# Kernel tuning notes

Measured on AMD Instinct MI355X. Metric: run time of the kernel, lower is better.

## Reference

```python
import jax, jax.numpy as jnp
import numpy as np

B, T, D_MODEL = 2, 2048, 1024
N_HEAD, D_HEAD = 16, 64
EPS = 1e-5


def setup_inputs() -> dict:
    key = jax.random.key(0)
    ks = jax.random.split(key, 6)
    s = 0.02  # init scale
    x = jax.random.normal(ks[0], (B, T, D_MODEL), jnp.float32)
    Wq = jax.random.normal(ks[1], (D_MODEL, N_HEAD * D_HEAD), jnp.float32) * s
    Wk = jax.random.normal(ks[2], (D_MODEL, N_HEAD * D_HEAD), jnp.float32) * s
    Wv = jax.random.normal(ks[3], (D_MODEL, N_HEAD * D_HEAD), jnp.float32) * s
    Wo = jax.random.normal(ks[4], (N_HEAD * D_HEAD, D_MODEL), jnp.float32) * s
    bo = jnp.zeros((D_MODEL,), jnp.float32)
    gamma = jnp.ones((D_MODEL,), jnp.float32)
    beta = jnp.zeros((D_MODEL,), jnp.float32)
    # causal mask: True = masked out (matches masked_fill semantics)
    mask = jnp.triu(jnp.ones((T, T), dtype=bool), k=1)[None, None]  # [1,1,T,T]
    return {"x": x, "Wq": Wq, "Wk": Wk, "Wv": Wv, "Wo": Wo, "bo": bo,
            "gamma": gamma, "beta": beta, "mask": mask}


def reference(x, Wq, Wk, Wv, Wo, bo, gamma, beta, mask):
    B_, T_, D = x.shape
    # pre-LayerNorm (biased variance, eps=1e-5, matching torch)
    mu = jnp.mean(x, axis=-1, keepdims=True)
    var = jnp.mean(jnp.square(x - mu), axis=-1, keepdims=True)
    xn = (x - mu) / jnp.sqrt(var + EPS) * gamma + beta
    # QKV projections (no bias)
    q = (xn @ Wq).reshape(B_, T_, N_HEAD, D_HEAD)
    k = (xn @ Wk).reshape(B_, T_, N_HEAD, D_HEAD)
    v = (xn @ Wv).reshape(B_, T_, N_HEAD, D_HEAD)
    scale = 1.0 / (D_HEAD ** 0.5)
    scores = jnp.einsum('bthd,bshd->bhts', q, k) * scale  # [B,H,T,T]
    scores = jnp.where(mask, -jnp.finfo(scores.dtype).max, scores)
    attn = jax.nn.softmax(scores, axis=-1)
    o = jnp.einsum('bhts,bshd->bthd', attn, v).reshape(B_, T_, N_HEAD * D_HEAD)
    out = o @ Wo + bo  # dropout is identity (eval / p=0)
    # pre_layernorm=True: residual uses the NORMALIZED x (faithful to source)
    return xn + out
```

## Files before the change

kernel.cpp:

```cpp
#include <hip/hip_runtime.h>
#include <hip/hip_bf16.h>

typedef unsigned short u16;
typedef __attribute__((ext_vector_type(8))) short bf16x8;
typedef __attribute__((ext_vector_type(4))) float f32x4;

#define T_SEQ 2048
#define DM 1024
#define NH 16
#define DH 64

__device__ __forceinline__ float bf2f(u16 u) {
  return __uint_as_float(((unsigned int)u) << 16);
}
__device__ __forceinline__ u16 f2bf(float f) {
  unsigned int u = __float_as_uint(f);
  u += 0x7fff + ((u >> 16) & 1);
  return (u16)(u >> 16);
}
__device__ __forceinline__ bool in_is_f32(const void* gamma) {
  return ((const u16*)gamma)[0] != 0x3F80;
}

__global__ __launch_bounds__(256) void ln_k(const void* __restrict__ x,
                                            const void* __restrict__ gamma,
                                            const void* __restrict__ beta,
                                            u16* __restrict__ xn,
                                            float2* __restrict__ stats) {
  bool f32 = in_is_f32(gamma);
  int row = blockIdx.x;
  int t = threadIdx.x;
  float v[4];
  if (f32) {
    float4 u = ((const float4*)((const float*)x + (size_t)row * DM))[t];
    v[0] = u.x; v[1] = u.y; v[2] = u.z; v[3] = u.w;
  } else {
    uint2 u = ((const uint2*)((const u16*)x + (size_t)row * DM))[t];
    v[0] = bf2f((u16)(u.x & 0xffff)); v[1] = bf2f((u16)(u.x >> 16));
    v[2] = bf2f((u16)(u.y & 0xffff)); v[3] = bf2f((u16)(u.y >> 16));
  }
  float s = v[0] + v[1] + v[2] + v[3];
  float ss = v[0]*v[0] + v[1]*v[1] + v[2]*v[2] + v[3]*v[3];
  #pragma unroll
  for (int m = 1; m < 64; m <<= 1) {
    s += __shfl_xor(s, m);
    ss += __shfl_xor(ss, m);
  }
  __shared__ float red[8];
  int wid = t >> 6;
  if ((t & 63) == 0) { red[wid] = s; red[4 + wid] = ss; }
  __syncthreads();
  float S = red[0] + red[1] + red[2] + red[3];
  float SS = red[4] + red[5] + red[6] + red[7];
  float mu = S * (1.0f / DM);
  float var = SS * (1.0f / DM) - mu * mu;
  float rstd = rsqrtf(var + 1e-5f);
  if (t == 0) stats[row] = make_float2(mu, rstd);
  float gv[4], bv[4];
  if (f32) {
    float4 ug = ((const float4*)gamma)[t];
    float4 ub = ((const float4*)beta)[t];
    gv[0] = ug.x; gv[1] = ug.y; gv[2] = ug.z; gv[3] = ug.w;
    bv[0] = ub.x; bv[1] = ub.y; bv[2] = ub.z; bv[3] = ub.w;
  } else {
    uint2 ug = ((const uint2*)gamma)[t];
    uint2 ub = ((const uint2*)beta)[t];
    gv[0] = bf2f((u16)(ug.x & 0xffff)); gv[1] = bf2f((u16)(ug.x >> 16));
    gv[2] = bf2f((u16)(ug.y & 0xffff)); gv[3] = bf2f((u16)(ug.y >> 16));
    bv[0] = bf2f((u16)(ub.x & 0xffff)); bv[1] = bf2f((u16)(ub.x >> 16));
    bv[2] = bf2f((u16)(ub.y & 0xffff)); bv[3] = bf2f((u16)(ub.y >> 16));
  }
  u16 o[4];
  #pragma unroll
  for (int i = 0; i < 4; i++) o[i] = f2bf((v[i] - mu) * rstd * gv[i] + bv[i]);
  uint2 w;
  w.x = (unsigned)o[0] | ((unsigned)o[1] << 16);
  w.y = (unsigned)o[2] | ((unsigned)o[3] << 16);
  *(uint2*)&xn[(size_t)row * DM + t * 4] = w;
}

__global__ __launch_bounds__(256) void transp_cvt(const void* __restrict__ W0,
                                                  const void* __restrict__ W1,
                                                  const void* __restrict__ W2,
                                                  const void* __restrict__ W3,
                                                  u16* __restrict__ out,
                                                  const void* __restrict__ gamma) {
  bool f32 = in_is_f32(gamma);
  int z = blockIdx.z;
  const void* in = (z == 0) ? W0 : (z == 1) ? W1 : (z == 2) ? W2 : W3;
  u16* dst0 = out + (size_t)z * 1024 * 1024;
  __shared__ __align__(16) u16 tile[64][72];
  int c0 = blockIdx.x * 64, r0 = blockIdx.y * 64;
  int t = threadIdx.x;
  int rr = t >> 2, seg = t & 3;
  u16 w[16];
  if (f32) {
    const float4* p = (const float4*)((const float*)in + (size_t)(r0 + rr) * 1024 + c0 + seg * 16);
    float4 q0 = p[0], q1 = p[1], q2 = p[2], q3 = p[3];
    w[0] = f2bf(q0.x);  w[1] = f2bf(q0.y);  w[2] = f2bf(q0.z);  w[3] = f2bf(q0.w);
    w[4] = f2bf(q1.x);  w[5] = f2bf(q1.y);  w[6] = f2bf(q1.z);  w[7] = f2bf(q1.w);
    w[8] = f2bf(q2.x);  w[9] = f2bf(q2.y);  w[10] = f2bf(q2.z); w[11] = f2bf(q2.w);
    w[12] = f2bf(q3.x); w[13] = f2bf(q3.y); w[14] = f2bf(q3.z); w[15] = f2bf(q3.w);
  } else {
    const u16* p = (const u16*)in + (size_t)(r0 + rr) * 1024 + c0 + seg * 16;
    bf16x8 a0 = *(const bf16x8*)p;
    bf16x8 a1 = *(const bf16x8*)(p + 8);
    #pragma unroll
    for (int i = 0; i < 8; i++) { w[i] = (u16)a0[i]; w[8 + i] = (u16)a1[i]; }
  }
  #pragma unroll
  for (int i = 0; i < 16; i++) tile[rr][seg * 16 + i] = w[i];
  __syncthreads();
  u16 vals[16];
  #pragma unroll
  for (int i = 0; i < 16; i++) vals[i] = tile[seg * 16 + i][rr];
  u16* dst = &dst0[(size_t)(c0 + rr) * 1024 + r0 + seg * 16];
  #pragma unroll
  for (int q = 0; q < 4; q++) {
    ushort4 p4;
    p4.x = vals[4 * q]; p4.y = vals[4 * q + 1]; p4.z = vals[4 * q + 2]; p4.w = vals[4 * q + 3];
    *(ushort4*)(dst + 4 * q) = p4;
  }
}

template<int TM, int LDA>
__global__ __launch_bounds__(256) void gemm_k(const u16* __restrict__ A,
                                              const u16* __restrict__ BT,
                                              u16* __restrict__ Cq,
                                              u16* __restrict__ vt,
                                              void* __restrict__ Cout,
                                              const void* __restrict__ bo,
                                              const void* __restrict__ x,
                                              const void* __restrict__ gamma,
                                              const void* __restrict__ beta,
                                              const float2* __restrict__ stats,
                                              int mode) {
  constexpr int NI = (TM == 128) ? 4 : 1;
  constexpr int NJ = (TM == 128) ? 4 : 8;
  constexpr int ACH = (TM == 128) ? 2 : 1;
  __shared__ __align__(16) u16 As[TM * 32];
  __shared__ __align__(16) u16 Bs[128 * 32];
  const int K = 1024;
  int tid = threadIdx.x;
  int lane = tid & 63, wid = tid >> 6;
  int wm = (TM == 128) ? (wid >> 1) : wid;
  int wn = (TM == 128) ? (wid & 1) : 0;
  int m0 = blockIdx.x * TM, n0 = blockIdx.y * 128;
  int quad = lane >> 4, lcol = lane & 15;
  bool vmode = (mode == 0) && (n0 >= 2048);

  f32x4 acc[NI][NJ];
  #pragma unroll
  for (int i = 0; i < NI; i++)
    #pragma unroll
    for (int j = 0; j < NJ; j++) acc[i][j] = (f32x4){0.f, 0.f, 0.f, 0.f};

  int srow = tid >> 2, scol = (tid & 3) * 8;
  const u16* Ag0 = A + (size_t)(m0 + srow) * LDA + scol;
  const u16* Ag1 = A + (size_t)(m0 + 64 + srow) * LDA + scol;
  const u16* Bg0 = BT + (size_t)(n0 + srow) * 1024 + scol;
  const u16* Bg1 = BT + (size_t)(n0 + 64 + srow) * 1024 + scol;

  uint4 pa0 = *(const uint4*)Ag0;
  uint4 pa1;
  if (ACH == 2) pa1 = *(const uint4*)Ag1;
  uint4 pb0 = *(const uint4*)Bg0;
  uint4 pb1 = *(const uint4*)Bg1;

  for (int k0 = 0; k0 < K; k0 += 32) {
    if (k0) __syncthreads();
    *(uint4*)(As + tid * 8) = pa0;
    if (ACH == 2) *(uint4*)(As + 2048 + tid * 8) = pa1;
    *(uint4*)(Bs + tid * 8) = pb0;
    *(uint4*)(Bs + 2048 + tid * 8) = pb1;
    __syncthreads();
    if (k0 + 32 < K) {
      pa0 = *(const uint4*)(Ag0 + k0 + 32);
      if (ACH == 2) pa1 = *(const uint4*)(Ag1 + k0 + 32);
      pb0 = *(const uint4*)(Bg0 + k0 + 32);
      pb1 = *(const uint4*)(Bg1 + k0 + 32);
    }
    bf16x8 af[NI], bfr[NJ];
    #pragma unroll
    for (int i = 0; i < NI; i++) {
      int row = (TM == 128) ? (wm * 64 + i * 16 + lcol) : (wm * 16 + lcol);
      af[i] = *(const bf16x8*)&As[row * 32 + quad * 8];
    }
    #pragma unroll
    for (int j = 0; j < NJ; j++) {
      int col = ((TM == 128) ? wn * 64 : 0) + j * 16 + lcol;
      bfr[j] = *(const bf16x8*)&Bs[col * 32 + quad * 8];
    }
    if (vmode) {
      #pragma unroll
      for (int i = 0; i < NI; i++)
        #pragma unroll
        for (int j = 0; j < NJ; j++)
          acc[i][j] = __builtin_amdgcn_mfma_f32_16x16x32_bf16(af[i], bfr[j], acc[i][j], 0, 0, 0);
    } else {
      #pragma unroll
      for (int i = 0; i < NI; i++)
        #pragma unroll
        for (int j = 0; j < NJ; j++)
          acc[i][j] = __builtin_amdgcn_mfma_f32_16x16x32_bf16(bfr[j], af[i], acc[i][j], 0, 0, 0);
    }
  }

  if (mode == 0) {
    if (!vmode) {
      #pragma unroll
      for (int i = 0; i < NI; i++) {
        int m = m0 + ((TM == 128) ? wm * 64 + i * 16 : wm * 16) + lcol;
        #pragma unroll
        for (int j = 0; j < NJ; j++) {
          int nb2 = n0 + ((TM == 128) ? wn * 64 : 0) + j * 16 + quad * 4;
          ushort4 p;
          p.x = f2bf(acc[i][j][0]); p.y = f2bf(acc[i][j][1]);
          p.z = f2bf(acc[i][j][2]); p.w = f2bf(acc[i][j][3]);
          *(ushort4*)&Cq[(size_t)m * 2048 + nb2] = p;
        }
      }
    } else {
      #pragma unroll
      for (int i = 0; i < NI; i++)
        #pragma unroll
        for (int j = 0; j < NJ; j++) {
          int c = n0 - 2048 + ((TM == 128) ? wn * 64 : 0) + j * 16 + lcol;
          int h = c >> 6, d = c & 63;
          int tb = m0 + ((TM == 128) ? wm * 64 + i * 16 : wm * 16) + quad * 4;
          int bb = tb >> 11, tt = tb & 2047;
          ushort4 p;
          p.x = f2bf(acc[i][j][0]); p.y = f2bf(acc[i][j][1]);
          p.z = f2bf(acc[i][j][2]); p.w = f2bf(acc[i][j][3]);
          *(ushort4*)&vt[((size_t)(bb * NH + h) * DH + d) * T_SEQ + tt] = p;
        }
    }
  } else {
    bool f32 = in_is_f32(gamma);
    #pragma unroll
    for (int i = 0; i < NI; i++) {
      int m = m0 + ((TM == 128) ? wm * 64 + i * 16 : wm * 16) + lcol;
      float2 st = stats[m];
      #pragma unroll
      for (int j = 0; j < NJ; j++) {
        int nb2 = n0 + ((TM == 128) ? wn * 64 : 0) + j * 16 + quad * 4;
        size_t idx = (size_t)m * DM + nb2;
        float g4[4], b4[4], bo4[4], x4[4];
        if (f32) {
          float4 g = *(const float4*)((const float*)gamma + nb2);
          float4 be = *(const float4*)((const float*)beta + nb2);
          float4 bb = *(const float4*)((const float*)bo + nb2);
          float4 xv = *(const float4*)((const float*)x + idx);
          g4[0]=g.x; g4[1]=g.y; g4[2]=g.z; g4[3]=g.w;
          b4[0]=be.x; b4[1]=be.y; b4[2]=be.z; b4[3]=be.w;
          bo4[0]=bb.x; bo4[1]=bb.y; bo4[2]=bb.z; bo4[3]=bb.w;
          x4[0]=xv.x; x4[1]=xv.y; x4[2]=xv.z; x4[3]=xv.w;
        } else {
          const u16* gp = (const u16*)gamma + nb2;
          const u16* bp = (const u16*)beta + nb2;
          const u16* op = (const u16*)bo + nb2;
          const u16* xp = (const u16*)x + idx;
          #pragma unroll
          for (int r = 0; r < 4; r++) {
            g4[r] = bf2f(gp[r]); b4[r] = bf2f(bp[r]);
            bo4[r] = bf2f(op[r]); x4[r] = bf2f(xp[r]);
          }
        }
        float o4[4];
        #pragma unroll
        for (int r = 0; r < 4; r++) {
          float xnv = (x4[r] - st.x) * st.y * g4[r] + b4[r];
          o4[r] = acc[i][j][r] + bo4[r] + xnv;
        }
        if (f32) {
          float4 o; o.x = o4[0]; o.y = o4[1]; o.z = o4[2]; o.w = o4[3];
          *(float4*)((float*)Cout + idx) = o;
        } else {
          ushort4 o;
          o.x = f2bf(o4[0]); o.y = f2bf(o4[1]); o.z = f2bf(o4[2]); o.w = f2bf(o4[3]);
          *(ushort4*)((u16*)Cout + idx) = o;
        }
      }
    }
  }
}

__global__ __launch_bounds__(256) void attn(const u16* __restrict__ qk,
                                            const u16* __restrict__ vt,
                                            u16* __restrict__ o) {
  __shared__ __align__(16) u16 Ks[64 * 72];
  __shared__ __align__(16) u16 Vs[64 * 72];
  __shared__ __align__(16) u16 Psm[4][16 * 72];
  int tid = threadIdx.x;
  int lane = tid & 63, wid = tid >> 6;
  int bh = blockIdx.y;
  int b = bh >> 4, h = bh & 15;
  int quad = lane >> 4, lcol = lane & 15;
  int r0 = tid >> 3, seg8 = (tid & 7) * 8;

  const u16* Kbase = qk + (size_t)(b * T_SEQ) * 2048 + 1024 + h * DH;
  const u16* Vbase = vt + (size_t)(b * NH + h) * DH * T_SEQ;

  #pragma unroll
  for (int pi = 0; pi < 2; pi++) {
    int qt = pi ? (int)blockIdx.x : 31 - (int)blockIdx.x;
    int q0 = qt * 64 + wid * 16;
    const u16* qrow = qk + ((size_t)(b * T_SEQ) + q0 + lcol) * 2048 + h * DH + quad * 8;
    bf16x8 qa0 = *(const bf16x8*)(qrow);
    bf16x8 qa1 = *(const bf16x8*)(qrow + 32);

    f32x4 Oacc[4];
    #pragma unroll
    for (int jd = 0; jd < 4; jd++) Oacc[jd] = (f32x4){0.f, 0.f, 0.f, 0.f};
    float lpart[4] = {0.f, 0.f, 0.f, 0.f};
    int ktmax = qt * 64;

    uint4 kp0 = *(const uint4*)(Kbase + (size_t)r0 * 2048 + seg8);
    uint4 kp1 = *(const uint4*)(Kbase + (size_t)(r0 + 32) * 2048 + seg8);
    uint4 vp0 = *(const uint4*)(Vbase + (size_t)r0 * 2048 + seg8);
    uint4 vp1 = *(const uint4*)(Vbase + (size_t)(r0 + 32) * 2048 + seg8);

    for (int kt = 0; kt <= ktmax; kt += 64) {
      __syncthreads();
      *(uint4*)&Ks[r0 * 72 + seg8] = kp0;
      *(uint4*)&Ks[(r0 + 32) * 72 + seg8] = kp1;
      *(uint4*)&Vs[r0 * 72 + seg8] = vp0;
      *(uint4*)&Vs[(r0 + 32) * 72 + seg8] = vp1;
      __syncthreads();
      if (kt < ktmax) {
        int kn = kt + 64;
        kp0 = *(const uint4*)(Kbase + (size_t)(kn + r0) * 2048 + seg8);
        kp1 = *(const uint4*)(Kbase + (size_t)(kn + r0 + 32) * 2048 + seg8);
        vp0 = *(const uint4*)(Vbase + (size_t)r0 * 2048 + kn + seg8);
        vp1 = *(const uint4*)(Vbase + (size_t)(r0 + 32) * 2048 + kn + seg8);
      }
      f32x4 S[4];
      #pragma unroll
      for (int j = 0; j < 4; j++) {
        bf16x8 kb0 = *(const bf16x8*)&Ks[(j * 16 + lcol) * 72 + quad * 8];
        bf16x8 kb1 = *(const bf16x8*)&Ks[(j * 16 + lcol) * 72 + 32 + quad * 8];
        f32x4 s = (f32x4){0.f, 0.f, 0.f, 0.f};
        s = __builtin_amdgcn_mfma_f32_16x16x32_bf16(qa0, kb0, s, 0, 0, 0);
        s = __builtin_amdgcn_mfma_f32_16x16x32_bf16(qa1, kb1, s, 0, 0, 0);
        S[j] = s;
      }
      if (kt < ktmax) {
        #pragma unroll
        for (int r = 0; r < 4; r++) {
          float rs = 0.f;
          #pragma unroll
          for (int j = 0; j < 4; j++) {
            float p = __expf(S[j][r] * 0.125f);
            S[j][r] = p;
            rs += p;
          }
          lpart[r] += rs;
        }
      } else {
        #pragma unroll
        for (int r = 0; r < 4; r++) {
          int qg = q0 + quad * 4 + r;
          float rs = 0.f;
          #pragma unroll
          for (int j = 0; j < 4; j++) {
            int key = kt + j * 16 + lcol;
            float p = (key <= qg) ? __expf(S[j][r] * 0.125f) : 0.f;
            S[j][r] = p;
            rs += p;
          }
          lpart[r] += rs;
        }
      }
      #pragma unroll
      for (int j = 0; j < 4; j++)
        #pragma unroll
        for (int r = 0; r < 4; r++)
          Psm[wid][(quad * 4 + r) * 72 + j * 16 + lcol] = f2bf(S[j][r]);
      #pragma unroll
      for (int s = 0; s < 2; s++) {
        bf16x8 pa = *(const bf16x8*)&Psm[wid][lcol * 72 + s * 32 + quad * 8];
        #pragma unroll
        for (int jd = 0; jd < 4; jd++) {
          bf16x8 vb = *(const bf16x8*)&Vs[(jd * 16 + lcol) * 72 + s * 32 + quad * 8];
          Oacc[jd] = __builtin_amdgcn_mfma_f32_16x16x32_bf16(pa, vb, Oacc[jd], 0, 0, 0);
        }
      }
    }
    #pragma unroll
    for (int r = 0; r < 4; r++) {
      float rs = lpart[r];
      rs += __shfl_xor(rs, 1);
      rs += __shfl_xor(rs, 2);
      rs += __shfl_xor(rs, 4);
      rs += __shfl_xor(rs, 8);
      float inv = 1.0f / rs;
      int qg = q0 + quad * 4 + r;
      size_t rowbase = ((size_t)(b * T_SEQ) + qg) * 2048 + h * DH;
      #pragma unroll
      for (int jd = 0; jd < 4; jd++)
        o[rowbase + jd * 16 + lcol] = f2bf(Oacc[jd][r] * inv);
    }
  }
}

extern "C" void kernel_launch(void* const* d_in, const int* in_sizes, int n_in,
                              void* d_out, int out_size, void* d_ws, size_t ws_size,
                              hipStream_t stream) {
  (void)in_sizes; (void)n_in; (void)out_size; (void)ws_size;
  const void* x     = d_in[0];
  const void* Wq    = d_in[1];
  const void* Wk    = d_in[2];
  const void* Wv    = d_in[3];
  const void* Wo    = d_in[4];
  const void* bo    = d_in[5];
  const void* gamma = d_in[6];
  const void* beta  = d_in[7];

  u16* ws = (u16*)d_ws;
  u16* xn  = ws;
  u16* qkb = xn + (size_t)4096 * 1024;
  u16* vt  = qkb + (size_t)4096 * 2048;
  u16* WT  = vt + (size_t)2 * 16 * 64 * 2048;
  float2* stats = (float2*)(WT + (size_t)4096 * 1024);
  u16* WoT = WT + (size_t)3 * 1024 * 1024;

  ln_k<<<4096, 256, 0, stream>>>(x, gamma, beta, xn, stats);

  transp_cvt<<<dim3(16, 16, 4), 256, 0, stream>>>(Wq, Wk, Wv, Wo, WT, gamma);

  gemm_k<128, 1024><<<dim3(32, 24), 256, 0, stream>>>(xn, WT, qkb, vt, nullptr,
                                                      nullptr, nullptr, gamma,
                                                      nullptr, nullptr, 0);

  attn<<<dim3(16, 32), 256, 0, stream>>>(qkb, vt, qkb);

  gemm_k<64, 2048><<<dim3(64, 8), 256, 0, stream>>>(qkb, WoT, nullptr, nullptr,
                                                    d_out, bo, x, gamma, beta,
                                                    stats, 1);
}
```

Measured before the change: 235.7 us.

## Split attention key tile across waves and keep P in registers via transposed MFMA

The attention block now splits each 64-key tile across its four waves instead of splitting the queries. Each wave computes S transposed (K as the A operand, Q as B) so the exp'd probabilities land directly in the 16x16x16 MFMA operand layout for P·V. This removes the per-wave P round trip through shared memory. The cost is that each wave now holds partial O accumulators for all 64 queries, which means a cross-wave reduction through shared memory, with extra syncs, at the end. Register use roughly quadruples for Oacc, which may reduce occupancy.

```diff
diff --git a/kernel.cpp b/kernel.cpp
--- a/kernel.cpp
+++ b/kernel.cpp
@@ -3,6 +3,7 @@
 
 typedef unsigned short u16;
 typedef __attribute__((ext_vector_type(8))) short bf16x8;
+typedef __attribute__((ext_vector_type(4))) short bf16x4;
 typedef __attribute__((ext_vector_type(4))) float f32x4;
 
 #define T_SEQ 2048
@@ -20,6 +21,16 @@
 }
 __device__ __forceinline__ bool in_is_f32(const void* gamma) {
   return ((const u16*)gamma)[0] != 0x3F80;
+}
+__device__ __forceinline__ f32x4 mfma16(bf16x4 a, bf16x4 b, f32x4 c) {
+#if __has_builtin(__builtin_amdgcn_mfma_f32_16x16x16bf16_1k)
+  return __builtin_amdgcn_mfma_f32_16x16x16bf16_1k(a, b, c, 0, 0, 0);
+#else
+  f32x4 d;
+  asm volatile("v_mfma_f32_16x16x16_bf16 %0, %1, %2, %3\n\ts_nop 7\n\ts_nop 2"
+               : "=v"(d) : "v"(a), "v"(b), "v"(c));
+  return d;
+#endif
 }
 
 __global__ __launch_bounds__(256) void ln_k(const void* __restrict__ x,
@@ -288,9 +299,11 @@
 __global__ __launch_bounds__(256) void attn(const u16* __restrict__ qk,
                                             const u16* __restrict__ vt,
                                             u16* __restrict__ o) {
-  __shared__ __align__(16) u16 Ks[64 * 72];
-  __shared__ __align__(16) u16 Vs[64 * 72];
-  __shared__ __align__(16) u16 Psm[4][16 * 72];
+  __shared__ __align__(16) unsigned char smem[64 * 72 * 2 * 2];
+  __shared__ float Lbuf[4][4][16];
+  u16* Ks = (u16*)smem;
+  u16* Vs = Ks + 64 * 72;
+  float* Ob = (float*)smem;
   int tid = threadIdx.x;
   int lane = tid & 63, wid = tid >> 6;
   int bh = blockIdx.y;
@@ -303,102 +316,102 @@
 
   #pragma unroll
   for (int pi = 0; pi < 2; pi++) {
-    int qt = pi ? (int)blockIdx.x : 31 - (int)blockIdx.x;
-    int q0 = qt * 64 + wid * 16;
-    const u16* qrow = qk + ((size_t)(b * T_SEQ) + q0 + lcol) * 2048 + h * DH + quad * 8;
-    bf16x8 qa0 = *(const bf16x8*)(qrow);
-    bf16x8 qa1 = *(const bf16x8*)(qrow + 32);
-
-    f32x4 Oacc[4];
-    #pragma unroll
-    for (int jd = 0; jd < 4; jd++) Oacc[jd] = (f32x4){0.f, 0.f, 0.f, 0.f};
+    int qt64 = pi ? (int)blockIdx.x : 31 - (int)blockIdx.x;
+    int q0 = qt64 * 64;
+    bf16x8 Qf[4][2];
+    #pragma unroll
+    for (int qt = 0; qt < 4; qt++) {
+      const u16* qp = qk + ((size_t)(b * T_SEQ) + q0 + qt * 16 + lcol) * 2048 + h * DH + quad * 8;
+      Qf[qt][0] = *(const bf16x8*)(qp);
+      Qf[qt][1] = *(const bf16x8*)(qp + 32);
+    }
+    f32x4 Oacc[4][4];
+    #pragma unroll
+    for (int dt = 0; dt < 4; dt++)
+      #pragma unroll
+      for (int qt = 0; qt < 4; qt++) Oacc[dt][qt] = (f32x4){0.f, 0.f, 0.f, 0.f};
     float lpart[4] = {0.f, 0.f, 0.f, 0.f};
-    int ktmax = qt * 64;
+    int rmax = qt64;
 
     uint4 kp0 = *(const uint4*)(Kbase + (size_t)r0 * 2048 + seg8);
     uint4 kp1 = *(const uint4*)(Kbase + (size_t)(r0 + 32) * 2048 + seg8);
     uint4 vp0 = *(const uint4*)(Vbase + (size_t)r0 * 2048 + seg8);
     uint4 vp1 = *(const uint4*)(Vbase + (size_t)(r0 + 32) * 2048 + seg8);
 
-    for (int kt = 0; kt <= ktmax; kt += 64) {
+    for (int r = 0; r <= rmax; r++) {
       __syncthreads();
       *(uint4*)&Ks[r0 * 72 + seg8] = kp0;
       *(uint4*)&Ks[(r0 + 32) * 72 + seg8] = kp1;
       *(uint4*)&Vs[r0 * 72 + seg8] = vp0;
       *(uint4*)&Vs[(r0 + 32) * 72 + seg8] = vp1;
       __syncthreads();
-      if (kt < ktmax) {
-        int kn = kt + 64;
+      if (r < rmax) {
+        int kn = (r + 1) * 64;
         kp0 = *(const uint4*)(Kbase + (size_t)(kn + r0) * 2048 + seg8);
         kp1 = *(const uint4*)(Kbase + (size_t)(kn + r0 + 32) * 2048 + seg8);
         vp0 = *(const uint4*)(Vbase + (size_t)r0 * 2048 + kn + seg8);
         vp1 = *(const uint4*)(Vbase + (size_t)(r0 + 32) * 2048 + kn + seg8);
       }
-      f32x4 S[4];
-      #pragma unroll
-      for (int j = 0; j < 4; j++) {
-        bf16x8 kb0 = *(const bf16x8*)&Ks[(j * 16 + lcol) * 72 + quad * 8];
-        bf16x8 kb1 = *(const bf16x8*)&Ks[(j * 16 + lcol) * 72 + 32 + quad * 8];
+      bf16x8 ka0 = *(const bf16x8*)&Ks[(wid * 16 + lcol) * 72 + quad * 8];
+      bf16x8 ka1 = *(const bf16x8*)&Ks[(wid * 16 + lcol) * 72 + 32 + quad * 8];
+      bf16x4 va[4];
+      #pragma unroll
+      for (int dt = 0; dt < 4; dt++)
+        va[dt] = *(const bf16x4*)&Vs[(dt * 16 + lcol) * 72 + wid * 16 + quad * 4];
+      #pragma unroll
+      for (int qt = 0; qt < 4; qt++) {
         f32x4 s = (f32x4){0.f, 0.f, 0.f, 0.f};
-        s = __builtin_amdgcn_mfma_f32_16x16x32_bf16(qa0, kb0, s, 0, 0, 0);
-        s = __builtin_amdgcn_mfma_f32_16x16x32_bf16(qa1, kb1, s, 0, 0, 0);
-        S[j] = s;
+        s = __builtin_amdgcn_mfma_f32_16x16x32_bf16(ka0, Qf[qt][0], s, 0, 0, 0);
+        s = __builtin_amdgcn_mfma_f32_16x16x32_bf16(ka1, Qf[qt][1], s, 0, 0, 0);
+        bf16x4 pb;
+        float rs = 0.f;
+        if (r < rmax) {
+          #pragma unroll
+          for (int i = 0; i < 4; i++) {
+            float p = __expf(s[i] * 0.125f);
+            rs += p;
+            pb[i] = (short)f2bf(p);
+          }
+        } else {
+          int qloc = qt * 16 + lcol;
+          #pragma unroll
+          for (int i = 0; i < 4; i++) {
+            int kloc = wid * 16 + quad * 4 + i;
+            float p = (kloc <= qloc) ? __expf(s[i] * 0.125f) : 0.f;
+            rs += p;
+            pb[i] = (short)f2bf(p);
+          }
+        }
+        lpart[qt] += rs;
+        #pragma unroll
+        for (int dt = 0; dt < 4; dt++)
+          Oacc[dt][qt] = mfma16(va[dt], pb, Oacc[dt][qt]);
       }
-      if (kt < ktmax) {
-        #pragma unroll
-        for (int r = 0; r < 4; r++) {
-          float rs = 0.f;
-          #pragma unroll
-          for (int j = 0; j < 4; j++) {
-            float p = __expf(S[j][r] * 0.125f);
-            S[j][r] = p;
-            rs += p;
-          }
-          lpart[r] += rs;
-        }
-      } else {
-        #pragma unroll
-        for (int r = 0; r < 4; r++) {
-          int qg = q0 + quad * 4 + r;
-          float rs = 0.f;
-          #pragma unroll
-          for (int j = 0; j < 4; j++) {
-            int key = kt + j * 16 + lcol;
-            float p = (key <= qg) ? __expf(S[j][r] * 0.125f) : 0.f;
-            S[j][r] = p;
-            rs += p;
-          }
-          lpart[r] += rs;
-        }
+    }
+    #pragma unroll
+    for (int qt = 0; qt < 4; qt++) {
+      float rsum = lpart[qt];
+      rsum += __shfl_xor(rsum, 16);
+      rsum += __shfl_xor(rsum, 32);
+      if (lane < 16) Lbuf[wid][qt][lane] = rsum;
+    }
+    for (int dt = 0; dt < 4; dt++) {
+      __syncthreads();
+      #pragma unroll
+      for (int qt = 0; qt < 4; qt++)
+        #pragma unroll
+        for (int rg = 0; rg < 4; rg++)
+          Ob[wid * 1088 + (quad * 4 + rg) * 68 + qt * 16 + lcol] = Oacc[dt][qt][rg];
+      __syncthreads();
+      #pragma unroll
+      for (int p = 0; p < 4; p++) {
+        int q = p * 16 + (tid >> 4), d = tid & 15;
+        float ssum = Ob[d * 68 + q] + Ob[1088 + d * 68 + q] +
+                     Ob[2176 + d * 68 + q] + Ob[3264 + d * 68 + q];
+        float l = Lbuf[0][q >> 4][q & 15] + Lbuf[1][q >> 4][q & 15] +
+                  Lbuf[2][q >> 4][q & 15] + Lbuf[3][q >> 4][q & 15];
+        o[((size_t)(b * T_SEQ) + q0 + q) * 2048 + h * DH + dt * 16 + d] = f2bf(ssum / l);
       }
-      #pragma unroll
-      for (int j = 0; j < 4; j++)
-        #pragma unroll
-        for (int r = 0; r < 4; r++)
-          Psm[wid][(quad * 4 + r) * 72 + j * 16 + lcol] = f2bf(S[j][r]);
-      #pragma unroll
-      for (int s = 0; s < 2; s++) {
-        bf16x8 pa = *(const bf16x8*)&Psm[wid][lcol * 72 + s * 32 + quad * 8];
-        #pragma unroll
-        for (int jd = 0; jd < 4; jd++) {
-          bf16x8 vb = *(const bf16x8*)&Vs[(jd * 16 + lcol) * 72 + s * 32 + quad * 8];
-          Oacc[jd] = __builtin_amdgcn_mfma_f32_16x16x32_bf16(pa, vb, Oacc[jd], 0, 0, 0);
-        }
-      }
-    }
-    #pragma unroll
-    for (int r = 0; r < 4; r++) {
-      float rs = lpart[r];
-      rs += __shfl_xor(rs, 1);
-      rs += __shfl_xor(rs, 2);
-      rs += __shfl_xor(rs, 4);
-      rs += __shfl_xor(rs, 8);
-      float inv = 1.0f / rs;
-      int qg = q0 + quad * 4 + r;
-      size_t rowbase = ((size_t)(b * T_SEQ) + qg) * 2048 + h * DH;
-      #pragma unroll
-      for (int jd = 0; jd < 4; jd++)
-        o[rowbase + jd * 16 + lcol] = f2bf(Oacc[jd][r] * inv);
     }
   }
 }
```

Result: no change. 234.8 us (-0.4%).
